# Optimization experiments

Hardware: AMD Instinct MI355X
Metric: run time of the kernel (lower is better)

## Reference

```python
import jax, jax.numpy as jnp
import numpy as np

DN = ('NCDHW', 'OIDHW', 'NCDHW')  # conv dimension numbers for 3D conv in torch layout
EPS = 1e-14


def setup_inputs() -> dict:
    key = jax.random.key(0)
    k1, k2 = jax.random.split(key)
    # xs: [B, C, D, H, W]
    xs = jax.random.normal(k1, (16, 128, 24, 24, 24), dtype=jnp.float32)
    # feature_vectors (prototypes): [num_features, C, w_1, h_1, L_1]
    feature_vectors = jax.random.normal(k2, (128, 128, 3, 3, 3), dtype=jnp.float32)
    return {"xs": xs, "feature_vectors": feature_vectors}


def reference(xs, feature_vectors):
    F_, C, kd, kh, kw = feature_vectors.shape
    # ||x_patch||^2: the original convolves xs**2 with all-ones weights of shape
    # [F, C, kd, kh, kw], producing F identical channels. We compute a single
    # sum-pool channel (same math) and let broadcasting supply the F channels.
    ones = jnp.ones((1, C, kd, kh, kw), dtype=xs.dtype)
    xs_squared_l2 = jax.lax.conv_general_dilated(
        xs * xs, ones, window_strides=(1, 1, 1), padding='VALID',
        dimension_numbers=DN)  # [B, 1, D', H', W']
    # ||p||^2 per prototype: [F, 1, 1, 1]
    ps_squared_l2 = jnp.sum(feature_vectors * feature_vectors,
                            axis=(1, 2, 3, 4)).reshape(-1, 1, 1, 1)
    # <x_patch, p>: the real weighted conv. [B, F, D', H', W']
    xs_conv = jax.lax.conv_general_dilated(
        xs, feature_vectors, window_strides=(1, 1, 1), padding='VALID',
        dimension_numbers=DN)
    distance = xs_squared_l2 + ps_squared_l2 - 2.0 * xs_conv
    return jnp.sqrt(jnp.abs(distance) + EPS)
```

## Files before the change

### kernel.cpp

```cpp
#include <hip/hip_runtime.h>
#include <hip/hip_bf16.h>

typedef __attribute__((ext_vector_type(8))) __bf16 bf16x8;
typedef __attribute__((ext_vector_type(2))) __bf16 bf16x2;
typedef __attribute__((ext_vector_type(4))) float f32x4;

#define B_   16
#define C_   128
#define DIM  24
#define F_   128
#define OD   22
#define OS   (OD*OD*OD)
#define SPB  (DIM*DIM*DIM)
#define K_   3456
#define M_   (B_*OS)
#define OUTN (B_*F_*OS)

__device__ __forceinline__ void async16(const void* g, void* l) {
  __builtin_amdgcn_global_load_lds(
      (const __attribute__((address_space(1))) unsigned int*)g,
      (__attribute__((address_space(3))) unsigned int*)l, 16, 0, 0);
}

__global__ __launch_bounds__(256) void prep_x(const float* __restrict__ xs,
                                              __bf16* __restrict__ xt,
                                              float* __restrict__ s1) {
  __shared__ float tile[C_ * 97];
  __shared__ float red[192];
  const int blk = blockIdx.x;
  const int yg = blk % 6;
  const int t2 = blk / 6;
  const int z = t2 % DIM;
  const int b = t2 / DIM;
  const int t = threadIdx.x;
  const float* src = xs + (size_t)b * C_ * SPB + z * (DIM * DIM) + yg * 96;
  for (int it = 0; it < 12; ++it) {
    int idx = it * 256 + t;
    int c = idx / 24, f4 = idx - c * 24;
    const float4 v = *(const float4*)(src + (size_t)c * SPB + f4 * 4);
    float* d = &tile[c * 97 + f4 * 4];
    d[0] = v.x; d[1] = v.y; d[2] = v.z; d[3] = v.w;
  }
  __syncthreads();
  size_t obase = ((size_t)b * SPB + z * (DIM * DIM) + yg * 96) * C_;
  for (int it = 0; it < 24; ++it) {
    int idx = it * 256 + t;
    int c2 = idx & 63, x = idx >> 6;
    bf16x2 v;
    v[0] = (__bf16)tile[(2 * c2) * 97 + x];
    v[1] = (__bf16)tile[(2 * c2 + 1) * 97 + x];
    *(bf16x2*)&xt[obase + (size_t)x * C_ + 2 * c2] = v;
  }
  if (t < 192) {
    int g = t / 96, p = t - g * 96;
    float s = 0.f;
    for (int c = g; c < C_; c += 2) {
      float v = tile[c * 97 + p];
      s += v * v;
    }
    red[g * 96 + p] = s;
  }
  __syncthreads();
  if (t < 96)
    s1[((size_t)b * SPB + z * (DIM * DIM) + yg * 96) + t] = red[t] + red[96 + t];
}

__global__ void prep_w(const float* __restrict__ fv, __bf16* __restrict__ Wt,
                       float* __restrict__ psq) {
  __shared__ float tile[K_];
  const int f = blockIdx.x;
  const float* src = fv + (size_t)f * K_;
  float part = 0.f;
  for (int idx = threadIdx.x; idx < K_; idx += 256) {
    float v = src[idx];
    tile[idx] = v;
    part += v * v;
  }
  __syncthreads();
  for (int idx = threadIdx.x; idx < K_; idx += 256) {
    int c = idx & 127, off = idx >> 7;
    Wt[(size_t)f * K_ + idx] = (__bf16)tile[c * 27 + off];
  }
  for (int o = 32; o > 0; o >>= 1) part += __shfl_down(part, o, 64);
  __shared__ float red[4];
  int w = threadIdx.x >> 6, l = threadIdx.x & 63;
  if (l == 0) red[w] = part;
  __syncthreads();
  if (threadIdx.x == 0) psq[f] = red[0] + red[1] + red[2] + red[3];
}

__global__ void pool_sq(const float* __restrict__ s1, float* __restrict__ xsq) {
  int i = blockIdx.x * 256 + threadIdx.x;
  if (i >= M_) return;
  int ow = i % OD;
  int t = i / OD;
  int oh = t % OD; t /= OD;
  int od = t % OD;
  int b = t / OD;
  const float* p = s1 + ((b * DIM + od) * DIM + oh) * DIM + ow;
  float s = 0.f;
#pragma unroll
  for (int dz = 0; dz < 3; ++dz)
#pragma unroll
    for (int dy = 0; dy < 3; ++dy)
#pragma unroll
      for (int dx = 0; dx < 3; ++dx)
        s += p[dz * 576 + dy * 24 + dx];
  xsq[i] = s;
}

__global__ __launch_bounds__(256) void l2gemm(
    const __bf16* __restrict__ xt, const __bf16* __restrict__ Wt,
    const float* __restrict__ xsq, const float* __restrict__ psq,
    float* __restrict__ out) {
  __shared__ __align__(16) __bf16 Wl[2][128 * 64];
  __shared__ __align__(16) __bf16 Pl[2][128 * 64];
  const int t = threadIdx.x;
  const int l = t & 63, w = t >> 6;
  const int quad = l >> 4, lan = l & 15;
  const int e = t & 7, r0 = t >> 3;
  const int esw = (e ^ (r0 & 7)) * 8;

  const int nwg = gridDim.x;
  const int orig = blockIdx.x;
  const int xcd = orig & 7, lo = orig >> 3;
  const int q = nwg >> 3, r = nwg & 7;
  const int mt = (xcd < r ? xcd * (q + 1) : r * (q + 1) + (xcd - r) * q) + lo;

  int sb[4];
#pragma unroll
  for (int p = 0; p < 4; ++p) {
    int m = mt * 128 + r0 + 32 * p;
    int b = m / OS;
    int s = m - b * OS;
    int od = s / (OD * OD);
    int s2 = s - od * (OD * OD);
    int oh = s2 / OD;
    int ow = s2 - oh * OD;
    sb[p] = b * SPB + od * 576 + oh * 24 + ow;
  }

  f32x4 acc[4][4];
#pragma unroll
  for (int i = 0; i < 4; ++i)
#pragma unroll
    for (int n = 0; n < 4; ++n) acc[i][n] = (f32x4){0.f, 0.f, 0.f, 0.f};

  const int wm = (w >> 1) * 64;
  const int wn = (w & 1) * 64;
  const int wrow = w * 8;

  auto stage = [&](int kt, int buf) {
    int off = kt >> 1;
    int dz = off / 9;
    int rem = off - dz * 9;
    int dy = rem / 3;
    int dx = rem - dy * 3;
    int doff = dz * 576 + dy * 24 + dx;
    int c0 = (kt & 1) << 6;
    __bf16* wl = &Wl[buf][wrow * 64];
    __bf16* pl = &Pl[buf][wrow * 64];
#pragma unroll
    for (int p = 0; p < 4; ++p) {
      const __bf16* gp = xt + (((size_t)(sb[p] + doff)) << 7) + c0 + esw;
      async16(gp, pl + (size_t)(32 * p) * 64);
      const __bf16* gw = Wt + (size_t)(r0 + 32 * p) * K_ + kt * 64 + esw;
      async16(gw, wl + (size_t)(32 * p) * 64);
    }
  };

  stage(0, 0);
  __syncthreads();
  int cur = 0;
#pragma unroll 1
  for (int kt = 0; kt < 54; ++kt) {
    if (kt < 53) stage(kt + 1, cur ^ 1);
    const __bf16* Wc = &Wl[cur][0];
    const __bf16* Pc = &Pl[cur][0];
#pragma unroll
    for (int kk = 0; kk < 2; ++kk) {
      bf16x8 a[4], bb[4];
      const int swz = (((kk * 4 + quad) ^ (lan & 7))) * 8;
#pragma unroll
      for (int i = 0; i < 4; ++i)
        a[i] = *(const bf16x8*)&Wc[(wm + i * 16 + lan) * 64 + swz];
#pragma unroll
      for (int n = 0; n < 4; ++n)
        bb[n] = *(const bf16x8*)&Pc[(wn + n * 16 + lan) * 64 + swz];
#pragma unroll
      for (int i = 0; i < 4; ++i)
#pragma unroll
        for (int n = 0; n < 4; ++n)
          acc[i][n] = __builtin_amdgcn_mfma_f32_16x16x32_bf16(a[i], bb[n],
                                                              acc[i][n], 0, 0, 0);
    }
    __syncthreads();
    cur ^= 1;
  }

  int mb[4];
  float xv[4];
#pragma unroll
  for (int n = 0; n < 4; ++n) {
    int m = mt * 128 + wn + n * 16 + lan;
    int b = m / OS;
    int s = m - b * OS;
    mb[n] = b * (F_ * OS) + s;
    xv[n] = xsq[m];
  }
#pragma unroll
  for (int i = 0; i < 4; ++i) {
#pragma unroll
    for (int r2 = 0; r2 < 4; ++r2) {
      int f = wm + i * 16 + quad * 4 + r2;
      float pq = psq[f];
#pragma unroll
      for (int n = 0; n < 4; ++n) {
        float d = xv[n] + pq - 2.0f * acc[i][n][r2];
        out[mb[n] + f * OS] = sqrtf(fabsf(d) + 1e-14f);
      }
    }
  }
}

__global__ void l2conv_direct(const float* __restrict__ xs,
                              const float* __restrict__ fv,
                              float* __restrict__ out) {
  int i = blockIdx.x * 256 + threadIdx.x;
  if (i >= OUTN) return;
  int s = i % OS;
  int t2 = i / OS;
  int f = t2 & 127;
  int b = t2 >> 7;
  int od = s / (OD * OD);
  int s2 = s - od * (OD * OD);
  int oh = s2 / OD;
  int ow = s2 - oh * OD;
  const float* xp = xs + (size_t)b * C_ * SPB + od * 576 + oh * 24 + ow;
  const float* wp = fv + (size_t)f * K_;
  float dot = 0.f, xq = 0.f, pq = 0.f;
  for (int c = 0; c < C_; ++c) {
    const float* xpc = xp + (size_t)c * SPB;
    const float* wpc = wp + c * 27;
#pragma unroll
    for (int o = 0; o < 27; ++o) {
      int dz = o / 9;
      int ry = o - dz * 9;
      int dy = ry / 3;
      int dx = ry - dy * 3;
      float xv = xpc[dz * 576 + dy * 24 + dx];
      float wv = wpc[o];
      dot += xv * wv;
      xq += xv * xv;
      pq += wv * wv;
    }
  }
  out[i] = sqrtf(fabsf(xq + pq - 2.f * dot) + 1e-14f);
}

extern "C" void kernel_launch(void* const* d_in, const int* in_sizes, int n_in,
                              void* d_out, int out_size, void* d_ws,
                              size_t ws_size, hipStream_t stream) {
  const float* xs = (const float*)d_in[0];
  const float* fv = (const float*)d_in[1];
  float* out = (float*)d_out;

  const size_t xt_b  = (size_t)B_ * SPB * C_ * 2;
  const size_t wt_b  = (size_t)F_ * K_ * 2;
  const size_t s1_b  = (size_t)B_ * SPB * 4;
  const size_t xsq_b = (size_t)M_ * 4;
  const size_t psq_b = 512;
  if (ws_size < xt_b + wt_b + s1_b + xsq_b + psq_b) {
    l2conv_direct<<<(OUTN + 255) / 256, 256, 0, stream>>>(xs, fv, out);
    return;
  }
  char* p = (char*)d_ws;
  __bf16* xt = (__bf16*)p;          p += xt_b;
  __bf16* Wt = (__bf16*)p;          p += wt_b;
  float*  s1 = (float*)p;           p += s1_b;
  float*  xsq = (float*)p;          p += xsq_b;
  float*  psq = (float*)p;

  prep_x<<<B_ * DIM * DIM / 4, 256, 0, stream>>>(xs, xt, s1);
  prep_w<<<F_, 256, 0, stream>>>(fv, Wt, psq);
  pool_sq<<<(M_ + 255) / 256, 256, 0, stream>>>(s1, xsq);
  l2gemm<<<M_ / 128, 256, 0, stream>>>(xt, Wt, xsq, psq, out);
}
```

Measured before the change: 382.7 us.

## Widen GEMM tile to 256 rows with 512 threads and explicit async pipeline

The block now uses 512 threads (8 waves) and covers 256 output rows per workgroup, so each staged weight tile is shared by twice as many patch rows. The K loop replaces the single __syncthreads with manual vmcnt/lgkmcnt waits and barriers. The next-but-one stage is issued after the LDS fragments are read into registers, and s_setprio is raised around the MFMA block. The aim is more overlap of global-to-LDS loads with matrix math and less redundant weight traffic. The cost is a partial tail tile that needs clamped indices and masked stores, a larger LDS footprint, and fewer workgroups in the grid.

```diff
diff --git a/kernel.cpp b/kernel.cpp
--- a/kernel.cpp
+++ b/kernel.cpp
@@ -109,12 +109,12 @@
   xsq[i] = s;
 }
 
-__global__ __launch_bounds__(256) void l2gemm(
+__global__ __launch_bounds__(512, 2) void l2gemm(
     const __bf16* __restrict__ xt, const __bf16* __restrict__ Wt,
     const float* __restrict__ xsq, const float* __restrict__ psq,
     float* __restrict__ out) {
   __shared__ __align__(16) __bf16 Wl[2][128 * 64];
-  __shared__ __align__(16) __bf16 Pl[2][128 * 64];
+  __shared__ __align__(16) __bf16 Pl[2][256 * 64];
   const int t = threadIdx.x;
   const int l = t & 63, w = t >> 6;
   const int quad = l >> 4, lan = l & 15;
@@ -130,7 +130,8 @@
   int sb[4];
 #pragma unroll
   for (int p = 0; p < 4; ++p) {
-    int m = mt * 128 + r0 + 32 * p;
+    int m = mt * 256 + r0 + 64 * p;
+    if (m >= M_) m = M_ - 1;
     int b = m / OS;
     int s = m - b * OS;
     int od = s / (OD * OD);
@@ -146,9 +147,8 @@
 #pragma unroll
     for (int n = 0; n < 4; ++n) acc[i][n] = (f32x4){0.f, 0.f, 0.f, 0.f};
 
-  const int wm = (w >> 1) * 64;
-  const int wn = (w & 1) * 64;
-  const int wrow = w * 8;
+  const int wm = (w & 1) * 64;
+  const int wn = (w >> 1) * 64;
 
   auto stage = [&](int kt, int buf) {
     int off = kt >> 1;
@@ -158,51 +158,70 @@
     int dx = rem - dy * 3;
     int doff = dz * 576 + dy * 24 + dx;
     int c0 = (kt & 1) << 6;
-    __bf16* wl = &Wl[buf][wrow * 64];
-    __bf16* pl = &Pl[buf][wrow * 64];
+    __bf16* wl = &Wl[buf][0];
+    __bf16* pl = &Pl[buf][0];
+#pragma unroll
+    for (int it = 0; it < 2; ++it) {
+      const __bf16* gw = Wt + (size_t)(r0 + 64 * it) * K_ + kt * 64 + esw;
+      async16(gw, wl + (size_t)(8 * w + 64 * it) * 64);
+    }
 #pragma unroll
     for (int p = 0; p < 4; ++p) {
       const __bf16* gp = xt + (((size_t)(sb[p] + doff)) << 7) + c0 + esw;
-      async16(gp, pl + (size_t)(32 * p) * 64);
-      const __bf16* gw = Wt + (size_t)(r0 + 32 * p) * K_ + kt * 64 + esw;
-      async16(gw, wl + (size_t)(32 * p) * 64);
+      async16(gp, pl + (size_t)(8 * w + 64 * p) * 64);
     }
   };
 
   stage(0, 0);
-  __syncthreads();
-  int cur = 0;
+  stage(1, 1);
+
 #pragma unroll 1
   for (int kt = 0; kt < 54; ++kt) {
-    if (kt < 53) stage(kt + 1, cur ^ 1);
+    const int cur = kt & 1;
+    if (kt < 53) {
+      asm volatile("s_waitcnt vmcnt(6)" ::: "memory");
+    } else {
+      asm volatile("s_waitcnt vmcnt(0)" ::: "memory");
+    }
+    __builtin_amdgcn_s_barrier();
+    __builtin_amdgcn_sched_barrier(0);
     const __bf16* Wc = &Wl[cur][0];
     const __bf16* Pc = &Pl[cur][0];
+    bf16x8 a[2][4], bb[2][4];
 #pragma unroll
     for (int kk = 0; kk < 2; ++kk) {
-      bf16x8 a[4], bb[4];
-      const int swz = (((kk * 4 + quad) ^ (lan & 7))) * 8;
+      const int swz = ((kk * 4 + quad) ^ (lan & 7)) * 8;
 #pragma unroll
       for (int i = 0; i < 4; ++i)
-        a[i] = *(const bf16x8*)&Wc[(wm + i * 16 + lan) * 64 + swz];
+        a[kk][i] = *(const bf16x8*)&Wc[(wm + i * 16 + lan) * 64 + swz];
 #pragma unroll
       for (int n = 0; n < 4; ++n)
-        bb[n] = *(const bf16x8*)&Pc[(wn + n * 16 + lan) * 64 + swz];
+        bb[kk][n] = *(const bf16x8*)&Pc[(wn + n * 16 + lan) * 64 + swz];
+    }
+    asm volatile("s_waitcnt lgkmcnt(0)" ::: "memory");
+    __builtin_amdgcn_sched_barrier(0);
+    __builtin_amdgcn_s_barrier();
+    if (kt < 52) stage(kt + 2, cur);
+    __builtin_amdgcn_sched_barrier(0);
+    __builtin_amdgcn_s_setprio(1);
+#pragma unroll
+    for (int kk = 0; kk < 2; ++kk)
 #pragma unroll
       for (int i = 0; i < 4; ++i)
 #pragma unroll
         for (int n = 0; n < 4; ++n)
-          acc[i][n] = __builtin_amdgcn_mfma_f32_16x16x32_bf16(a[i], bb[n],
+          acc[i][n] = __builtin_amdgcn_mfma_f32_16x16x32_bf16(a[kk][i], bb[kk][n],
                                                               acc[i][n], 0, 0, 0);
-    }
-    __syncthreads();
-    cur ^= 1;
-  }
-
-  int mb[4];
+    __builtin_amdgcn_s_setprio(0);
+  }
+
+  int mb[4], mok[4];
   float xv[4];
 #pragma unroll
   for (int n = 0; n < 4; ++n) {
-    int m = mt * 128 + wn + n * 16 + lan;
+    int m = mt * 256 + wn + n * 16 + lan;
+    mok[n] = (m < M_);
+    if (m >= M_) m = M_ - 1;
     int b = m / OS;
     int s = m - b * OS;
     mb[n] = b * (F_ * OS) + s;
@@ -216,8 +235,10 @@
       float pq = psq[f];
 #pragma unroll
       for (int n = 0; n < 4; ++n) {
-        float d = xv[n] + pq - 2.0f * acc[i][n][r2];
-        out[mb[n] + f * OS] = sqrtf(fabsf(d) + 1e-14f);
+        if (mok[n]) {
+          float d = xv[n] + pq - 2.0f * acc[i][n][r2];
+          out[mb[n] + f * OS] = sqrtf(fabsf(d) + 1e-14f);
+        }
       }
     }
   }
@@ -284,5 +305,5 @@
   prep_x<<<B_ * DIM * DIM / 4, 256, 0, stream>>>(xs, xt, s1);
   prep_w<<<F_, 256, 0, stream>>>(fv, Wt, psq);
   pool_sq<<<(M_ + 255) / 256, 256, 0, stream>>>(s1, xsq);
-  l2gemm<<<M_ / 128, 256, 0, stream>>>(xt, Wt, xsq, psq, out);
-}
+  l2gemm<<<(M_ + 255) / 256, 512, 0, stream>>>(xt, Wt, xsq, psq, out);
+}
```

New measurement: 410.9 us. 7.4% more time.

## Switch implicit-GEMM to FP8 operands with register-direct single-wave tiles

Applied to the files above, without the earlier changes.

Input activations and prototype weights are now quantized to FP8 e4m3 instead of bf16, and the GEMM uses the fp8 16x16x32 MFMA. The LDS staging is gone: each single-wave workgroup loads A fragments from a pre-swizzled weight layout and B fragments straight from global memory into registers, double-buffered in registers. This halves operand bytes and removes LDS traffic and barriers. In exchange it loses the LDS reuse across waves and adds substantial quantization error in the dot product, which the squared-distance subtraction can amplify.

```diff
diff --git a/kernel.cpp b/kernel.cpp
--- a/kernel.cpp
+++ b/kernel.cpp
@@ -1,9 +1,9 @@
 #include <hip/hip_runtime.h>
 #include <hip/hip_bf16.h>
-
-typedef __attribute__((ext_vector_type(8))) __bf16 bf16x8;
+#include <hip/hip_fp8.h>
+
+typedef __attribute__((ext_vector_type(4))) float f32x4;
 typedef __attribute__((ext_vector_type(2))) __bf16 bf16x2;
-typedef __attribute__((ext_vector_type(4))) float f32x4;
 
 #define B_   16
 #define C_   128
@@ -15,15 +15,14 @@
 #define K_   3456
 #define M_   (B_*OS)
 #define OUTN (B_*F_*OS)
-
-__device__ __forceinline__ void async16(const void* g, void* l) {
-  __builtin_amdgcn_global_load_lds(
-      (const __attribute__((address_space(1))) unsigned int*)g,
-      (__attribute__((address_space(3))) unsigned int*)l, 16, 0, 0);
+#define NSL  108
+
+__device__ __forceinline__ unsigned char f2fp8(float v) {
+  return __hip_fp8_e4m3(v).__x;
 }
 
 __global__ __launch_bounds__(256) void prep_x(const float* __restrict__ xs,
-                                              __bf16* __restrict__ xt,
+                                              unsigned char* __restrict__ xt,
                                               float* __restrict__ s1) {
   __shared__ float tile[C_ * 97];
   __shared__ float red[192];
@@ -43,13 +42,17 @@
   }
   __syncthreads();
   size_t obase = ((size_t)b * SPB + z * (DIM * DIM) + yg * 96) * C_;
-  for (int it = 0; it < 24; ++it) {
+  for (int it = 0; it < 6; ++it) {
     int idx = it * 256 + t;
-    int c2 = idx & 63, x = idx >> 6;
-    bf16x2 v;
-    v[0] = (__bf16)tile[(2 * c2) * 97 + x];
-    v[1] = (__bf16)tile[(2 * c2 + 1) * 97 + x];
-    *(bf16x2*)&xt[obase + (size_t)x * C_ + 2 * c2] = v;
+    int s = idx & 15, x = idx >> 4;
+    unsigned int w0 = 0, w1 = 0;
+#pragma unroll
+    for (int j = 0; j < 4; ++j)
+      w0 |= ((unsigned int)f2fp8(tile[(8 * s + j) * 97 + x])) << (8 * j);
+#pragma unroll
+    for (int j = 0; j < 4; ++j)
+      w1 |= ((unsigned int)f2fp8(tile[(8 * s + 4 + j) * 97 + x])) << (8 * j);
+    *(uint2*)&xt[obase + (size_t)x * C_ + s * 8] = make_uint2(w0, w1);
   }
   if (t < 192) {
     int g = t / 96, p = t - g * 96;
@@ -65,7 +68,8 @@
     s1[((size_t)b * SPB + z * (DIM * DIM) + yg * 96) + t] = red[t] + red[96 + t];
 }
 
-__global__ void prep_w(const float* __restrict__ fv, __bf16* __restrict__ Wt,
+__global__ void prep_w(const float* __restrict__ fv,
+                       unsigned char* __restrict__ Wt2,
                        float* __restrict__ psq) {
   __shared__ float tile[K_];
   const int f = blockIdx.x;
@@ -77,9 +81,13 @@
     part += v * v;
   }
   __syncthreads();
+  const int g = f >> 4, fl = f & 15;
   for (int idx = threadIdx.x; idx < K_; idx += 256) {
-    int c = idx & 127, off = idx >> 7;
-    Wt[(size_t)f * K_ + idx] = (__bf16)tile[c * 27 + off];
+    int tap = idx >> 7, c = idx & 127;
+    int kk = c >> 5, q = (c >> 3) & 3, j = c & 7;
+    int s = tap * 4 + kk;
+    int l = fl + (q << 4);
+    Wt2[((size_t)(s * 8 + g) * 64 + l) * 8 + j] = f2fp8(tile[c * 27 + tap]);
   }
   for (int o = 32; o > 0; o >>= 1) part += __shfl_down(part, o, 64);
   __shared__ float red[4];
@@ -109,114 +117,92 @@
   xsq[i] = s;
 }
 
-__global__ __launch_bounds__(256) void l2gemm(
-    const __bf16* __restrict__ xt, const __bf16* __restrict__ Wt,
+__global__ __launch_bounds__(64, 2) void l2gemm(
+    const unsigned char* __restrict__ xt, const unsigned char* __restrict__ Wt2,
     const float* __restrict__ xsq, const float* __restrict__ psq,
     float* __restrict__ out) {
-  __shared__ __align__(16) __bf16 Wl[2][128 * 64];
-  __shared__ __align__(16) __bf16 Pl[2][128 * 64];
-  const int t = threadIdx.x;
-  const int l = t & 63, w = t >> 6;
-  const int quad = l >> 4, lan = l & 15;
-  const int e = t & 7, r0 = t >> 3;
-  const int esw = (e ^ (r0 & 7)) * 8;
+  const int l = threadIdx.x;
+  const int lan = l & 15, quad = l >> 4;
 
   const int nwg = gridDim.x;
   const int orig = blockIdx.x;
   const int xcd = orig & 7, lo = orig >> 3;
   const int q = nwg >> 3, r = nwg & 7;
   const int mt = (xcd < r ? xcd * (q + 1) : r * (q + 1) + (xcd - r) * q) + lo;
-
-  int sb[4];
-#pragma unroll
-  for (int p = 0; p < 4; ++p) {
-    int m = mt * 128 + r0 + 32 * p;
+  const int m0 = mt * 64;
+
+  int vof[4];
+#pragma unroll
+  for (int n = 0; n < 4; ++n) {
+    int m = m0 + n * 16 + lan;
     int b = m / OS;
     int s = m - b * OS;
     int od = s / (OD * OD);
     int s2 = s - od * (OD * OD);
     int oh = s2 / OD;
     int ow = s2 - oh * OD;
-    sb[p] = b * SPB + od * 576 + oh * 24 + ow;
-  }
-
-  f32x4 acc[4][4];
-#pragma unroll
-  for (int i = 0; i < 4; ++i)
-#pragma unroll
-    for (int n = 0; n < 4; ++n) acc[i][n] = (f32x4){0.f, 0.f, 0.f, 0.f};
-
-  const int wm = (w >> 1) * 64;
-  const int wn = (w & 1) * 64;
-  const int wrow = w * 8;
-
-  auto stage = [&](int kt, int buf) {
-    int off = kt >> 1;
-    int dz = off / 9;
-    int rem = off - dz * 9;
+    vof[n] = (b * SPB + od * 576 + oh * 24 + ow) * 128 + quad * 8;
+  }
+  const int aof = l * 8;
+
+  f32x4 acc[8][4];
+#pragma unroll
+  for (int g = 0; g < 8; ++g)
+#pragma unroll
+    for (int n = 0; n < 4; ++n) acc[g][n] = (f32x4){0.f, 0.f, 0.f, 0.f};
+
+  long A0[8], B0[4], A1[8], B1[4];
+
+  auto LD = [&](long* A, long* B, int s) {
+    int tap = s >> 2, k0 = (s & 3) << 5;
+    int dz = tap / 9;
+    int rem = tap - dz * 9;
     int dy = rem / 3;
     int dx = rem - dy * 3;
-    int doff = dz * 576 + dy * 24 + dx;
-    int c0 = (kt & 1) << 6;
-    __bf16* wl = &Wl[buf][wrow * 64];
-    __bf16* pl = &Pl[buf][wrow * 64];
-#pragma unroll
-    for (int p = 0; p < 4; ++p) {
-      const __bf16* gp = xt + (((size_t)(sb[p] + doff)) << 7) + c0 + esw;
-      async16(gp, pl + (size_t)(32 * p) * 64);
-      const __bf16* gw = Wt + (size_t)(r0 + 32 * p) * K_ + kt * 64 + esw;
-      async16(gw, wl + (size_t)(32 * p) * 64);
-    }
+    const unsigned char* xp = xt + (dz * 576 + dy * 24 + dx) * 128 + k0;
+    const unsigned char* ap = Wt2 + (size_t)s * 4096 + aof;
+#pragma unroll
+    for (int g = 0; g < 8; ++g) A[g] = *(const long*)(ap + g * 512);
+#pragma unroll
+    for (int n = 0; n < 4; ++n) B[n] = *(const long*)(xp + vof[n]);
   };
-
-  stage(0, 0);
-  __syncthreads();
-  int cur = 0;
+  auto MM = [&](long* A, long* B) {
+#pragma unroll
+    for (int g = 0; g < 8; ++g)
+#pragma unroll
+      for (int n = 0; n < 4; ++n)
+        acc[g][n] = __builtin_amdgcn_mfma_f32_16x16x32_fp8_fp8(A[g], B[n],
+                                                               acc[g][n], 0, 0, 0);
+  };
+
+  LD(A0, B0, 0);
 #pragma unroll 1
-  for (int kt = 0; kt < 54; ++kt) {
-    if (kt < 53) stage(kt + 1, cur ^ 1);
-    const __bf16* Wc = &Wl[cur][0];
-    const __bf16* Pc = &Pl[cur][0];
-#pragma unroll
-    for (int kk = 0; kk < 2; ++kk) {
-      bf16x8 a[4], bb[4];
-      const int swz = (((kk * 4 + quad) ^ (lan & 7))) * 8;
-#pragma unroll
-      for (int i = 0; i < 4; ++i)
-        a[i] = *(const bf16x8*)&Wc[(wm + i * 16 + lan) * 64 + swz];
-#pragma unroll
-      for (int n = 0; n < 4; ++n)
-        bb[n] = *(const bf16x8*)&Pc[(wn + n * 16 + lan) * 64 + swz];
-#pragma unroll
-      for (int i = 0; i < 4; ++i)
-#pragma unroll
-        for (int n = 0; n < 4; ++n)
-          acc[i][n] = __builtin_amdgcn_mfma_f32_16x16x32_bf16(a[i], bb[n],
-                                                              acc[i][n], 0, 0, 0);
-    }
-    __syncthreads();
-    cur ^= 1;
+  for (int s = 0; s < NSL; s += 2) {
+    LD(A1, B1, s + 1);
+    MM(A0, B0);
+    if (s + 2 < NSL) LD(A0, B0, s + 2);
+    MM(A1, B1);
   }
 
   int mb[4];
   float xv[4];
 #pragma unroll
   for (int n = 0; n < 4; ++n) {
-    int m = mt * 128 + wn + n * 16 + lan;
+    int m = m0 + n * 16 + lan;
     int b = m / OS;
     int s = m - b * OS;
     mb[n] = b * (F_ * OS) + s;
     xv[n] = xsq[m];
   }
 #pragma unroll
-  for (int i = 0; i < 4; ++i) {
+  for (int g = 0; g < 8; ++g) {
 #pragma unroll
     for (int r2 = 0; r2 < 4; ++r2) {
-      int f = wm + i * 16 + quad * 4 + r2;
+      int f = g * 16 + quad * 4 + r2;
       float pq = psq[f];
 #pragma unroll
       for (int n = 0; n < 4; ++n) {
-        float d = xv[n] + pq - 2.0f * acc[i][n][r2];
+        float d = xv[n] + pq - 2.0f * acc[g][n][r2];
         out[mb[n] + f * OS] = sqrtf(fabsf(d) + 1e-14f);
       }
     }
@@ -265,8 +251,8 @@
   const float* fv = (const float*)d_in[1];
   float* out = (float*)d_out;
 
-  const size_t xt_b  = (size_t)B_ * SPB * C_ * 2;
-  const size_t wt_b  = (size_t)F_ * K_ * 2;
+  const size_t xt_b  = (size_t)B_ * SPB * C_;
+  const size_t wt_b  = (size_t)F_ * K_;
   const size_t s1_b  = (size_t)B_ * SPB * 4;
   const size_t xsq_b = (size_t)M_ * 4;
   const size_t psq_b = 512;
@@ -275,14 +261,14 @@
     return;
   }
   char* p = (char*)d_ws;
-  __bf16* xt = (__bf16*)p;          p += xt_b;
-  __bf16* Wt = (__bf16*)p;          p += wt_b;
-  float*  s1 = (float*)p;           p += s1_b;
-  float*  xsq = (float*)p;          p += xsq_b;
-  float*  psq = (float*)p;
+  unsigned char* xt = (unsigned char*)p;  p += xt_b;
+  unsigned char* Wt2 = (unsigned char*)p; p += wt_b;
+  float* s1 = (float*)p;                  p += s1_b;
+  float* xsq = (float*)p;                 p += xsq_b;
+  float* psq = (float*)p;
 
   prep_x<<<B_ * DIM * DIM / 4, 256, 0, stream>>>(xs, xt, s1);
-  prep_w<<<F_, 256, 0, stream>>>(fv, Wt, psq);
+  prep_w<<<F_, 256, 0, stream>>>(fv, Wt2, psq);
   pool_sq<<<(M_ + 255) / 256, 256, 0, stream>>>(s1, xsq);
-  l2gemm<<<M_ / 128, 256, 0, stream>>>(xt, Wt, xsq, psq, out);
-}
+  l2gemm<<<M_ / 64, 64, 0, stream>>>(xt, Wt2, xsq, psq, out);
+}
```

New measurement: 524.3 us. +37.0%, slower.
